# Optimization experiments

Hardware: AMD Instinct MI355X
Metric: run time of the kernel (lower is better)

## Reference

```python
import jax, jax.numpy as jnp
import numpy as np

N, E = 50000, 400000
IN_CH, HID, HEADS, EDGE_DIM = 128, 64, 4, 3
NEG_SLOPE = 0.2


def gatv2_conv(x, src, dst, edge_attr, Wl, Wr, We, att, bias):
    # x: [N, F_in]; Wl/Wr: [H*C, F_in]; We: [H*C, edge_dim]; att: [H, C]; bias: [C]
    H, C = att.shape
    n = x.shape[0]
    xl = (x @ Wl.T).reshape(n, H, C)   # source-side transform (lin_l)
    xr = (x @ Wr.T).reshape(n, H, C)   # target-side transform (lin_r)
    e = (edge_attr @ We.T).reshape(-1, H, C)
    z = jax.nn.leaky_relu(xl[src] + xr[dst] + e, NEG_SLOPE)  # [E,H,C]
    alpha = jnp.einsum('ehc,hc->eh', z, att)                 # [E,H]
    # segment softmax over incoming edges per destination node
    amax = jax.ops.segment_max(alpha, dst, num_segments=n)
    alpha = jnp.exp(alpha - amax[dst])
    denom = jax.ops.segment_sum(alpha, dst, num_segments=n)
    alpha = alpha / (denom[dst] + 1e-16)
    msg = xl[src] * alpha[:, :, None]                        # [E,H,C]
    out = jax.ops.segment_sum(msg, dst, num_segments=n)      # [N,H,C]
    return out.mean(axis=1) + bias                           # concat=False -> head mean


def setup_inputs() -> dict:
    key = jax.random.key(0)
    ks = jax.random.split(key, 16)
    s = 0.1
    return {
        'x': jax.random.normal(ks[0], (N, IN_CH), jnp.float32),
        'edge_index': jax.random.randint(ks[1], (2, E), 0, N, jnp.int32),
        'edge_attr': jax.random.normal(ks[2], (E, EDGE_DIM), jnp.float32),
        'Wl1': jax.random.normal(ks[3], (HEADS * HID, IN_CH), jnp.float32) * s,
        'Wr1': jax.random.normal(ks[4], (HEADS * HID, IN_CH), jnp.float32) * s,
        'We1': jax.random.normal(ks[5], (HEADS * HID, EDGE_DIM), jnp.float32) * s,
        'att1': jax.random.normal(ks[6], (HEADS, HID), jnp.float32) * s,
        'b1': jnp.zeros((HID,), jnp.float32),
        'Wl2': jax.random.normal(ks[7], (HEADS * HID, HID), jnp.float32) * s,
        'Wr2': jax.random.normal(ks[8], (HEADS * HID, HID), jnp.float32) * s,
        'We2': jax.random.normal(ks[9], (HEADS * HID, EDGE_DIM), jnp.float32) * s,
        'att2': jax.random.normal(ks[10], (HEADS, HID), jnp.float32) * s,
        'b2': jnp.zeros((HID,), jnp.float32),
        'prelu_w': jnp.full((HID,), 0.25, jnp.float32),
    }


def reference(x, edge_index, edge_attr, Wl1, Wr1, We1, att1, b1, Wl2, Wr2, We2, att2, b2, prelu_w):
    src, dst = edge_index[0], edge_index[1]
    h = gatv2_conv(x, src, dst, edge_attr, Wl1, Wr1, We1, att1, b1)
    h = gatv2_conv(h, src, dst, edge_attr, Wl2, Wr2, We2, att2, b2)
    return jnp.where(h >= 0, h, prelu_w * h)  # PReLU, per-channel weight
```

## Files before the change

kernel.cpp:

```cpp
#include <hip/hip_runtime.h>
#include <hip/hip_bf16.h>

#define HC 256

typedef __attribute__((ext_vector_type(8))) short bf16x8;
typedef __attribute__((ext_vector_type(4))) float f32x4;
typedef __attribute__((ext_vector_type(2))) float f32x2;

__device__ __forceinline__ void gl_lds16(const void* g, void* l) {
  __builtin_amdgcn_global_load_lds(
      (const __attribute__((address_space(1))) unsigned int*)g,
      (__attribute__((address_space(3))) unsigned int*)l, 16, 0, 0);
}

__device__ __forceinline__ void cast_w_one(const float* Wl, const float* Wr,
                                           ushort* WT, int F, int idx) {
  int col = idx / F, f = idx - col * F;
  float v = (col < 256) ? Wl[col * F + f] : Wr[(col - 256) * F + f];
  __hip_bfloat16 h = __float2bfloat16(v);
  WT[(size_t)col * F + f] = *(ushort*)&h;
}

__global__ void k_weights_hist(const float* __restrict__ Wl1, const float* __restrict__ Wr1,
                               ushort* __restrict__ WT1, const float* __restrict__ Wl2,
                               const float* __restrict__ Wr2, ushort* __restrict__ WT2,
                               const int* __restrict__ ei, int* __restrict__ deg, int E_) {
  int idx = blockIdx.x * blockDim.x + threadIdx.x;
  const int t1 = 512 * 128, t2 = 512 * 64;
  if (idx < t1) {
    cast_w_one(Wl1, Wr1, WT1, 128, idx);
  } else if (idx < t1 + t2) {
    cast_w_one(Wl2, Wr2, WT2, 64, idx - t1);
  } else {
    int e = idx - t1 - t2;
    if (e < E_) atomicAdd(&deg[ei[E_ + e]], 1);
  }
}

template <int F>
__global__ __launch_bounds__(256) void gemm_mfma(const ushort* __restrict__ A,
                                                 const ushort* __restrict__ WT,
                                                 ushort* __restrict__ xlb,
                                                 ushort* __restrict__ xrb, int n_nodes) {
  constexpr int NSTEP = F / 64;
  constexpr int SM = (2 * NSTEP * 8192 > 17408) ? 2 * NSTEP * 8192 : 17408;
  __shared__ __align__(16) ushort smem[SM];
  const int tid = threadIdx.x;
  const int wv = tid >> 6, lane = tid & 63;
  const int m16 = lane & 15, quad = lane >> 4;
  const int col0 = blockIdx.x * 128;
  const int row0 = blockIdx.y * 128;
  const int wm = (wv >> 1) * 64, wn = (wv & 1) * 64;

  f32x4 acc[4][4];
#pragma unroll
  for (int i = 0; i < 4; ++i)
#pragma unroll
    for (int j = 0; j < 4; ++j) acc[i][j] = (f32x4){0.f, 0.f, 0.f, 0.f};

  auto load_step = [&](int s) {
    ushort* As = smem + s * 16384;
    ushort* Bs = As + 8192;
    const int khat = s * 64;
#pragma unroll
    for (int t = 0; t < 4; ++t) {
      const int sl16 = tid + 256 * t;
      const int row = sl16 >> 3, sl = sl16 & 7;
      const int gch = sl ^ (row & 7);
      const int grow = row0 + row;
      if (grow < n_nodes)
        gl_lds16(A + (size_t)grow * F + khat + gch * 8, As + sl16 * 8);
      gl_lds16(WT + (size_t)(col0 + row) * F + khat + gch * 8, Bs + sl16 * 8);
    }
  };

  auto mfma_step = [&](int s) {
    ushort* As = smem + s * 16384;
    ushort* Bs = As + 8192;
#pragma unroll
    for (int kh = 0; kh < 2; ++kh) {
      bf16x8 af[4], bf[4];
#pragma unroll
      for (int i = 0; i < 4; ++i) {
        const int row = wm + i * 16 + m16;
        const int slot = (kh * 4 + quad) ^ (row & 7);
        af[i] = *(bf16x8*)&As[row * 64 + slot * 8];
      }
#pragma unroll
      for (int j = 0; j < 4; ++j) {
        const int col = wn + j * 16 + m16;
        const int slot = (kh * 4 + quad) ^ (col & 7);
        bf[j] = *(bf16x8*)&Bs[col * 64 + slot * 8];
      }
#pragma unroll
      for (int i = 0; i < 4; ++i)
#pragma unroll
        for (int j = 0; j < 4; ++j)
          acc[i][j] =
              __builtin_amdgcn_mfma_f32_16x16x32_bf16(af[i], bf[j], acc[i][j], 0, 0, 0);
    }
  };

  load_step(0);
  __syncthreads();
  if (NSTEP > 1) load_step(1);
  mfma_step(0);
  if (NSTEP > 1) {
    __syncthreads();
    mfma_step(1);
  }

  __syncthreads();
  ushort* Ct = smem;
#pragma unroll
  for (int i = 0; i < 4; ++i) {
#pragma unroll
    for (int r = 0; r < 4; ++r) {
      const int row = wm + i * 16 + quad * 4 + r;
#pragma unroll
      for (int j = 0; j < 4; ++j) {
        __hip_bfloat16 h = __float2bfloat16(acc[i][j][r]);
        Ct[row * 136 + wn + j * 16 + m16] = *(ushort*)&h;
      }
    }
  }
  __syncthreads();
  const bool is_xl = (col0 < 256);
  ushort* dst = is_xl ? xlb : xrb;
  const int cb = is_xl ? col0 : (col0 - 256);
  const int chunk = tid & 15;
#pragma unroll
  for (int it = 0; it < 8; ++it) {
    const int row = (tid >> 4) + 16 * it;
    const int grow = row0 + row;
    int4 v = *(int4*)&Ct[row * 136 + chunk * 8];
    if (grow < n_nodes)
      *(int4*)(dst + (size_t)grow * 256 + cb + chunk * 8) = v;
  }
}

__global__ void k_scan_local(const int* __restrict__ deg, int* __restrict__ rowstart,
                             int* __restrict__ partial, int n) {
  __shared__ int a[256], b[256];
  const int t = threadIdx.x;
  const int i = blockIdx.x * 256 + t;
  const int v = (i < n) ? deg[i] : 0;
  a[t] = v;
  __syncthreads();
  int* cur = a;
  int* nxt = b;
  for (int off = 1; off < 256; off <<= 1) {
    int x = cur[t];
    if (t >= off) x += cur[t - off];
    nxt[t] = x;
    __syncthreads();
    int* tmp = cur; cur = nxt; nxt = tmp;
  }
  const int incl = cur[t];
  if (i < n) rowstart[i] = incl - v;
  if (t == 255) partial[blockIdx.x] = incl;
}

__global__ void k_scan_partial(int* __restrict__ partial, int nblk,
                               float4* __restrict__ sea, int E_) {
  __shared__ int a[256], b[256];
  const int t = threadIdx.x;
  if (t < 8) sea[E_ + t] = make_float4(0.f, 0.f, 0.f, 0.f);
  const int v = (t < nblk) ? partial[t] : 0;
  a[t] = v;
  __syncthreads();
  int* cur = a;
  int* nxt = b;
  for (int off = 1; off < 256; off <<= 1) {
    int x = cur[t];
    if (t >= off) x += cur[t - off];
    nxt[t] = x;
    __syncthreads();
    int* tmp = cur; cur = nxt; nxt = tmp;
  }
  if (t < nblk) partial[t] = cur[t] - v;
}

__global__ void k_add_off(int* __restrict__ rowstart, int* __restrict__ cursor,
                          const int* __restrict__ partial, int n, int E_) {
  int i = blockIdx.x * blockDim.x + threadIdx.x;
  if (i < n) {
    int v = rowstart[i] + partial[i >> 8];
    rowstart[i] = v;
    cursor[i] = v;
  }
  if (i == 0) rowstart[n] = E_;
}

__global__ void k_prep(const float* __restrict__ x, ushort* __restrict__ A,
                       const int* __restrict__ ei, const float* __restrict__ ea,
                       int* __restrict__ cursor, float4* __restrict__ sea,
                       int n, int E_) {
  const int nx8 = n * 16;
  int idx = blockIdx.x * blockDim.x + threadIdx.x;
  if (idx < nx8) {
    const float4* xp = (const float4*)x + (size_t)idx * 2;
    float4 v0 = xp[0], v1 = xp[1];
    float vv[8] = {v0.x, v0.y, v0.z, v0.w, v1.x, v1.y, v1.z, v1.w};
    __align__(16) ushort hb[8];
#pragma unroll
    for (int j = 0; j < 8; ++j) {
      __hip_bfloat16 h = __float2bfloat16(vv[j]);
      hb[j] = *(ushort*)&h;
    }
    *(int4*)(A + (size_t)idx * 8) = *(int4*)hb;
  } else {
    int e = idx - nx8;
    if (e < E_) {
      int dst = ei[E_ + e];
      int pos = atomicAdd(&cursor[dst], 1);
      sea[pos] = make_float4(ea[e * 3], ea[e * 3 + 1], ea[e * 3 + 2],
                             __int_as_float(ei[e]));
    }
  }
}

__device__ __forceinline__ f32x2 vmax2(f32x2 a, f32x2 b) {
  return (f32x2){fmaxf(a.x, b.x), fmaxf(a.y, b.y)};
}
__device__ __forceinline__ f32x2 vmin2(f32x2 a, f32x2 b) {
  return (f32x2){fminf(a.x, b.x), fminf(a.y, b.y)};
}

__device__ __forceinline__ void edge_step(
    const ushort4& lu, const float4& eav, const f32x2* we0, const f32x2* we1,
    const f32x2* we2, const f32x2* at, const f32x2* xrl, f32x2& num01,
    f32x2& num23, float& den) {
  f32x2 lav0, lav1;
  lav0.x = __uint_as_float((unsigned)lu.x << 16);
  lav0.y = __uint_as_float((unsigned)lu.y << 16);
  lav1.x = __uint_as_float((unsigned)lu.z << 16);
  lav1.y = __uint_as_float((unsigned)lu.w << 16);
  const f32x2 zero = {0.f, 0.f};
  const f32x2 slope = {0.2f, 0.2f};
  f32x2 pv = zero;
#pragma unroll
  for (int j = 0; j < 2; ++j) {
    f32x2 la = (j == 0) ? lav0 : lav1;
    f32x2 ev = we0[j] * eav.x + we1[j] * eav.y + we2[j] * eav.z;
    f32x2 s = la + xrl[j] + ev;
    f32x2 z = vmax2(s, zero) + slope * vmin2(s, zero);
    pv = pv + z * at[j];
  }
  float p = pv.x + pv.y;
  p += __shfl_xor(p, 1);
  p += __shfl_xor(p, 2);
  p += __shfl_xor(p, 4);
  p += __shfl_xor(p, 8);
  const float w = __expf(p);
  den += w;
  num01 = num01 + (f32x2){w, w} * lav0;
  num23 = num23 + (f32x2){w, w} * lav1;
}

template <int MODE>
__global__ __launch_bounds__(64) void fused_attn(
    const ushort* __restrict__ xlb, const ushort* __restrict__ xrb,
    const int* __restrict__ rowstart, const float4* __restrict__ sea,
    const float* __restrict__ We, const float* __restrict__ att,
    const float* __restrict__ bias, const float* __restrict__ pw,
    float* __restrict__ out, ushort* __restrict__ outs, int n, int chunk) {
  const int lane = threadIdx.x;
  const int d0 = blockIdx.x * chunk;
  if (d0 >= n) return;
  const int d1 = min(d0 + chunk, n);

  f32x2 we0[2], we1[2], we2[2], at[2];
#pragma unroll
  for (int j = 0; j < 4; ++j) {
    int r = 4 * lane + j;
    ((float*)we0)[j] = We[r * 3 + 0];
    ((float*)we1)[j] = We[r * 3 + 1];
    ((float*)we2)[j] = We[r * 3 + 2];
    ((float*)at)[j] = att[r];
  }
  const float4 bias4 = ((const float4*)bias)[lane & 15];
  float4 pw4 = {0.f, 0.f, 0.f, 0.f};
  if (MODE == 1) pw4 = ((const float4*)pw)[lane & 15];
  const ushort4* xlb4 = (const ushort4*)xlb;

  for (int d = d0; d < d1; ++d) {
    const ushort4 xu = ((const ushort4*)xrb)[(unsigned)(d * 64) + lane];
    f32x2 xrl[2];
    xrl[0].x = __uint_as_float((unsigned)xu.x << 16);
    xrl[0].y = __uint_as_float((unsigned)xu.y << 16);
    xrl[1].x = __uint_as_float((unsigned)xu.z << 16);
    xrl[1].y = __uint_as_float((unsigned)xu.w << 16);

    int pos = rowstart[d];
    const int end = rowstart[d + 1];
    f32x2 num01 = {0.f, 0.f}, num23 = {0.f, 0.f};
    float den = 0.f;

    if (pos < end) {
      float4 e0 = sea[pos], e1 = sea[pos + 1], e2 = sea[pos + 2], e3 = sea[pos + 3];
      ushort4 g0 = xlb4[(unsigned)(__float_as_int(e0.w) * 64) + lane];
      ushort4 g1 = xlb4[(unsigned)(__float_as_int(e1.w) * 64) + lane];
      ushort4 g2 = xlb4[(unsigned)(__float_as_int(e2.w) * 64) + lane];
      ushort4 g3 = xlb4[(unsigned)(__float_as_int(e3.w) * 64) + lane];

      while (pos + 4 <= end) {
        ushort4 h0 = g0, h1 = g1, h2 = g2, h3 = g3;
        float4 f0 = e0, f1 = e1, f2 = e2, f3 = e3;
        if (pos + 4 < end) {
          f0 = sea[pos + 4];
          f1 = sea[pos + 5];
          f2 = sea[pos + 6];
          f3 = sea[pos + 7];
          h0 = xlb4[(unsigned)(__float_as_int(f0.w) * 64) + lane];
          h1 = xlb4[(unsigned)(__float_as_int(f1.w) * 64) + lane];
          h2 = xlb4[(unsigned)(__float_as_int(f2.w) * 64) + lane];
          h3 = xlb4[(unsigned)(__float_as_int(f3.w) * 64) + lane];
        }
        edge_step(g0, e0, we0, we1, we2, at, xrl, num01, num23, den);
        edge_step(g1, e1, we0, we1, we2, at, xrl, num01, num23, den);
        edge_step(g2, e2, we0, we1, we2, at, xrl, num01, num23, den);
        edge_step(g3, e3, we0, we1, we2, at, xrl, num01, num23, den);
        g0 = h0; g1 = h1; g2 = h2; g3 = h3;
        e0 = f0; e1 = f1; e2 = f2; e3 = f3;
        pos += 4;
      }
      const int rem = end - pos;
      if (rem > 0) edge_step(g0, e0, we0, we1, we2, at, xrl, num01, num23, den);
      if (rem > 1) edge_step(g1, e1, we0, we1, we2, at, xrl, num01, num23, den);
      if (rem > 2) edge_step(g2, e2, we0, we1, we2, at, xrl, num01, num23, den);
    }

    const float inv = 1.f / (den + 1e-16f);
    float4 r;
    r.x = num01.x * inv;
    r.y = num01.y * inv;
    r.z = num23.x * inv;
    r.w = num23.y * inv;
    r.x += __shfl_xor(r.x, 16);
    r.y += __shfl_xor(r.y, 16);
    r.z += __shfl_xor(r.z, 16);
    r.w += __shfl_xor(r.w, 16);
    r.x += __shfl_xor(r.x, 32);
    r.y += __shfl_xor(r.y, 32);
    r.z += __shfl_xor(r.z, 32);
    r.w += __shfl_xor(r.w, 32);
    if (lane < 16) {
      float o[4];
      o[0] = 0.25f * r.x + bias4.x;
      o[1] = 0.25f * r.y + bias4.y;
      o[2] = 0.25f * r.z + bias4.z;
      o[3] = 0.25f * r.w + bias4.w;
      if (MODE == 1) {
        const float pwv[4] = {pw4.x, pw4.y, pw4.z, pw4.w};
#pragma unroll
        for (int j = 0; j < 4; ++j) o[j] = (o[j] >= 0.f) ? o[j] : pwv[j] * o[j];
        ((float4*)out)[(size_t)d * 16 + lane] = make_float4(o[0], o[1], o[2], o[3]);
      } else {
        ushort hb[4];
#pragma unroll
        for (int j = 0; j < 4; ++j) {
          __hip_bfloat16 h = __float2bfloat16(o[j]);
          hb[j] = *(ushort*)&h;
        }
        *(ushort4*)(outs + (size_t)d * 64 + 4 * lane) =
            make_ushort4(hb[0], hb[1], hb[2], hb[3]);
      }
    }
  }
}

extern "C" void kernel_launch(void* const* d_in, const int* in_sizes, int n_in,
                              void* d_out, int out_size, void* d_ws, size_t ws_size,
                              hipStream_t stream) {
  const float* x    = (const float*)d_in[0];
  const int*   ei   = (const int*)d_in[1];
  const float* ea   = (const float*)d_in[2];
  const float* Wl1  = (const float*)d_in[3];
  const float* Wr1  = (const float*)d_in[4];
  const float* We1  = (const float*)d_in[5];
  const float* att1 = (const float*)d_in[6];
  const float* b1   = (const float*)d_in[7];
  const float* Wl2  = (const float*)d_in[8];
  const float* Wr2  = (const float*)d_in[9];
  const float* We2  = (const float*)d_in[10];
  const float* att2 = (const float*)d_in[11];
  const float* b2   = (const float*)d_in[12];
  const float* pw   = (const float*)d_in[13];
  const int N_ = in_sizes[0] / 128;
  const int E_ = in_sizes[1] / 2;
  float* out = (float*)d_out;

  char* w = (char*)d_ws;
  auto alloc = [&](size_t bytes) {
    char* p = w;
    w += (bytes + 255) & ~size_t(255);
    return p;
  };
  ushort* xlb      = (ushort*)alloc((size_t)N_ * 256 * 2);
  ushort* xrb      = (ushort*)alloc((size_t)N_ * 256 * 2);
  ushort* Ax       = (ushort*)alloc((size_t)N_ * 128 * 2);
  ushort* h2       = (ushort*)alloc((size_t)N_ * 64 * 2);
  float4* sea      = (float4*)alloc((size_t)(E_ + 8) * 16);
  int*    deg      = (int*)alloc((size_t)N_ * 4);
  int*    rowstart = (int*)alloc((size_t)(N_ + 1) * 4);
  int*    cursor   = (int*)alloc((size_t)N_ * 4);
  int*    partial  = (int*)alloc(256 * 4);
  ushort* WT1      = (ushort*)alloc((size_t)512 * 128 * 2);
  ushort* WT2      = (ushort*)alloc((size_t)512 * 64 * 2);

  hipMemsetAsync(deg, 0, (size_t)N_ * 4, stream);
  const int wtot = 512 * 128 + 512 * 64 + E_;
  k_weights_hist<<<(wtot + 255) / 256, 256, 0, stream>>>(Wl1, Wr1, WT1, Wl2, Wr2, WT2,
                                                         ei, deg, E_);

  const int nblk = (N_ + 255) / 256;
  k_scan_local<<<nblk, 256, 0, stream>>>(deg, rowstart, partial, N_);
  k_scan_partial<<<1, 256, 0, stream>>>(partial, nblk, sea, E_);
  k_add_off<<<nblk, 256, 0, stream>>>(rowstart, cursor, partial, N_, E_);
  const int ptot = N_ * 16 + E_;
  k_prep<<<(ptot + 255) / 256, 256, 0, stream>>>(x, Ax, ei, ea, cursor, sea, N_, E_);

  const dim3 GG(4, (N_ + 127) / 128);
  const int chunk = 2;
  const int FB = (N_ + chunk - 1) / chunk;

  gemm_mfma<128><<<GG, 256, 0, stream>>>(Ax, WT1, xlb, xrb, N_);
  fused_attn<0><<<FB, 64, 0, stream>>>(xlb, xrb, rowstart, sea, We1, att1,
                                       b1, pw, nullptr, h2, N_, chunk);
  gemm_mfma<64><<<GG, 256, 0, stream>>>(h2, WT2, xlb, xrb, N_);
  fused_attn<1><<<FB, 64, 0, stream>>>(xlb, xrb, rowstart, sea, We2, att2,
                                       b2, pw, out, nullptr, N_, chunk);
}
```

Before: 270.3 us.

## Stream edges across destination boundaries in fused attention with continuous prefetch

Reworks the fused attention kernel so a block walks one continuous stream of edges covering all its destinations. Each destination is finalized inline when the edge position reaches its row end, instead of draining and restarting the 4-deep gather pipeline per destination. Row starts are loaded once per block and broadcast with shuffles, and the next destination's xr row is prefetched. The per-block destination chunk is raised from 2 to 4, which gives fewer blocks with longer serial work and more divergent control flow around finalization.

```diff
diff --git a/kernel.cpp b/kernel.cpp
--- a/kernel.cpp
+++ b/kernel.cpp
@@ -227,6 +227,13 @@
   return (f32x2){fminf(a.x, b.x), fminf(a.y, b.y)};
 }
 
+__device__ __forceinline__ void expand_xr(const ushort4& xu, f32x2* xrl) {
+  xrl[0].x = __uint_as_float((unsigned)xu.x << 16);
+  xrl[0].y = __uint_as_float((unsigned)xu.y << 16);
+  xrl[1].x = __uint_as_float((unsigned)xu.z << 16);
+  xrl[1].y = __uint_as_float((unsigned)xu.w << 16);
+}
+
 __device__ __forceinline__ void edge_step(
     const ushort4& lu, const float4& eav, const f32x2* we0, const f32x2* we1,
     const f32x2* we2, const f32x2* at, const f32x2* xrl, f32x2& num01,
@@ -269,6 +276,7 @@
   const int d0 = blockIdx.x * chunk;
   if (d0 >= n) return;
   const int d1 = min(d0 + chunk, n);
+  const int nd = d1 - d0;
 
   f32x2 we0[2], we1[2], we2[2], at[2];
 #pragma unroll
@@ -283,91 +291,97 @@
   float4 pw4 = {0.f, 0.f, 0.f, 0.f};
   if (MODE == 1) pw4 = ((const float4*)pw)[lane & 15];
   const ushort4* xlb4 = (const ushort4*)xlb;
-
-  for (int d = d0; d < d1; ++d) {
-    const ushort4 xu = ((const ushort4*)xrb)[(unsigned)(d * 64) + lane];
-    f32x2 xrl[2];
-    xrl[0].x = __uint_as_float((unsigned)xu.x << 16);
-    xrl[0].y = __uint_as_float((unsigned)xu.y << 16);
-    xrl[1].x = __uint_as_float((unsigned)xu.z << 16);
-    xrl[1].y = __uint_as_float((unsigned)xu.w << 16);
-
-    int pos = rowstart[d];
-    const int end = rowstart[d + 1];
-    f32x2 num01 = {0.f, 0.f}, num23 = {0.f, 0.f};
-    float den = 0.f;
-
-    if (pos < end) {
-      float4 e0 = sea[pos], e1 = sea[pos + 1], e2 = sea[pos + 2], e3 = sea[pos + 3];
-      ushort4 g0 = xlb4[(unsigned)(__float_as_int(e0.w) * 64) + lane];
-      ushort4 g1 = xlb4[(unsigned)(__float_as_int(e1.w) * 64) + lane];
-      ushort4 g2 = xlb4[(unsigned)(__float_as_int(e2.w) * 64) + lane];
-      ushort4 g3 = xlb4[(unsigned)(__float_as_int(e3.w) * 64) + lane];
-
-      while (pos + 4 <= end) {
-        ushort4 h0 = g0, h1 = g1, h2 = g2, h3 = g3;
-        float4 f0 = e0, f1 = e1, f2 = e2, f3 = e3;
-        if (pos + 4 < end) {
-          f0 = sea[pos + 4];
-          f1 = sea[pos + 5];
-          f2 = sea[pos + 6];
-          f3 = sea[pos + 7];
-          h0 = xlb4[(unsigned)(__float_as_int(f0.w) * 64) + lane];
-          h1 = xlb4[(unsigned)(__float_as_int(f1.w) * 64) + lane];
-          h2 = xlb4[(unsigned)(__float_as_int(f2.w) * 64) + lane];
-          h3 = xlb4[(unsigned)(__float_as_int(f3.w) * 64) + lane];
+  const ushort4* xrb4 = (const ushort4*)xrb;
+
+  int rsv = 0;
+  if (lane <= nd) rsv = rowstart[d0 + lane];
+  int d = d0;
+  int pos = __shfl(rsv, 0);
+  const int fin = __shfl(rsv, nd);
+  int end_cur = __shfl(rsv, 1);
+
+  f32x2 xrl[2];
+  {
+    ushort4 xu0 = xrb4[(unsigned)(d0 * 64) + lane];
+    expand_xr(xu0, xrl);
+  }
+  ushort4 xu_nxt = xrb4[(unsigned)(min(d0 + 1, n - 1) * 64) + lane];
+  int d_pref = d0 + 2;
+
+  f32x2 num01 = {0.f, 0.f}, num23 = {0.f, 0.f};
+  float den = 0.f;
+
+#define FINALIZE_DST()                                                        \
+  do {                                                                        \
+    const float inv = 1.f / (den + 1e-16f);                                   \
+    float4 r;                                                                 \
+    r.x = num01.x * inv; r.y = num01.y * inv;                                 \
+    r.z = num23.x * inv; r.w = num23.y * inv;                                 \
+    r.x += __shfl_xor(r.x, 16); r.y += __shfl_xor(r.y, 16);                   \
+    r.z += __shfl_xor(r.z, 16); r.w += __shfl_xor(r.w, 16);                   \
+    r.x += __shfl_xor(r.x, 32); r.y += __shfl_xor(r.y, 32);                   \
+    r.z += __shfl_xor(r.z, 32); r.w += __shfl_xor(r.w, 32);                   \
+    if (lane < 16) {                                                          \
+      float o[4];                                                             \
+      o[0] = 0.25f * r.x + bias4.x; o[1] = 0.25f * r.y + bias4.y;             \
+      o[2] = 0.25f * r.z + bias4.z; o[3] = 0.25f * r.w + bias4.w;             \
+      if (MODE == 1) {                                                        \
+        const float pwv[4] = {pw4.x, pw4.y, pw4.z, pw4.w};                    \
+        _Pragma("unroll")                                                     \
+        for (int j = 0; j < 4; ++j) o[j] = (o[j] >= 0.f) ? o[j] : pwv[j] * o[j]; \
+        ((float4*)out)[(size_t)d * 16 + lane] = make_float4(o[0], o[1], o[2], o[3]); \
+      } else {                                                                \
+        ushort hb[4];                                                         \
+        _Pragma("unroll")                                                     \
+        for (int j = 0; j < 4; ++j) {                                         \
+          __hip_bfloat16 hh = __float2bfloat16(o[j]);                         \
+          hb[j] = *(ushort*)&hh;                                              \
+        }                                                                     \
+        *(ushort4*)(outs + (size_t)d * 64 + 4 * lane) =                       \
+            make_ushort4(hb[0], hb[1], hb[2], hb[3]);                         \
+      }                                                                       \
+    }                                                                         \
+    num01 = (f32x2){0.f, 0.f}; num23 = (f32x2){0.f, 0.f}; den = 0.f;          \
+    ++d;                                                                      \
+    end_cur = __shfl(rsv, d - d0 + 1);                                        \
+    expand_xr(xu_nxt, xrl);                                                   \
+    xu_nxt = xrb4[(unsigned)(min(d_pref, n - 1) * 64) + lane];                \
+    ++d_pref;                                                                 \
+  } while (0)
+
+  if (pos < fin) {
+    float4 e[4];
+    ushort4 g[4];
+#pragma unroll
+    for (int k = 0; k < 4; ++k) e[k] = sea[pos + k];
+#pragma unroll
+    for (int k = 0; k < 4; ++k)
+      g[k] = xlb4[(unsigned)(__float_as_int(e[k].w) * 64) + lane];
+
+    while (pos < fin) {
+      float4 f_[4];
+      ushort4 h_[4];
+#pragma unroll
+      for (int k = 0; k < 4; ++k) f_[k] = sea[pos + 4 + k];
+#pragma unroll
+      for (int k = 0; k < 4; ++k)
+        h_[k] = xlb4[(unsigned)(__float_as_int(f_[k].w) * 64) + lane];
+
+#pragma unroll
+      for (int k = 0; k < 4; ++k) {
+        const int p = pos + k;
+        if (p < fin) {
+          while (p == end_cur) FINALIZE_DST();
+          edge_step(g[k], e[k], we0, we1, we2, at, xrl, num01, num23, den);
         }
-        edge_step(g0, e0, we0, we1, we2, at, xrl, num01, num23, den);
-        edge_step(g1, e1, we0, we1, we2, at, xrl, num01, num23, den);
-        edge_step(g2, e2, we0, we1, we2, at, xrl, num01, num23, den);
-        edge_step(g3, e3, we0, we1, we2, at, xrl, num01, num23, den);
-        g0 = h0; g1 = h1; g2 = h2; g3 = h3;
-        e0 = f0; e1 = f1; e2 = f2; e3 = f3;
-        pos += 4;
       }
-      const int rem = end - pos;
-      if (rem > 0) edge_step(g0, e0, we0, we1, we2, at, xrl, num01, num23, den);
-      if (rem > 1) edge_step(g1, e1, we0, we1, we2, at, xrl, num01, num23, den);
-      if (rem > 2) edge_step(g2, e2, we0, we1, we2, at, xrl, num01, num23, den);
-    }
-
-    const float inv = 1.f / (den + 1e-16f);
-    float4 r;
-    r.x = num01.x * inv;
-    r.y = num01.y * inv;
-    r.z = num23.x * inv;
-    r.w = num23.y * inv;
-    r.x += __shfl_xor(r.x, 16);
-    r.y += __shfl_xor(r.y, 16);
-    r.z += __shfl_xor(r.z, 16);
-    r.w += __shfl_xor(r.w, 16);
-    r.x += __shfl_xor(r.x, 32);
-    r.y += __shfl_xor(r.y, 32);
-    r.z += __shfl_xor(r.z, 32);
-    r.w += __shfl_xor(r.w, 32);
-    if (lane < 16) {
-      float o[4];
-      o[0] = 0.25f * r.x + bias4.x;
-      o[1] = 0.25f * r.y + bias4.y;
-      o[2] = 0.25f * r.z + bias4.z;
-      o[3] = 0.25f * r.w + bias4.w;
-      if (MODE == 1) {
-        const float pwv[4] = {pw4.x, pw4.y, pw4.z, pw4.w};
-#pragma unroll
-        for (int j = 0; j < 4; ++j) o[j] = (o[j] >= 0.f) ? o[j] : pwv[j] * o[j];
-        ((float4*)out)[(size_t)d * 16 + lane] = make_float4(o[0], o[1], o[2], o[3]);
-      } else {
-        ushort hb[4];
-#pragma unroll
-        for (int j = 0; j < 4; ++j) {
-          __hip_bfloat16 h = __float2bfloat16(o[j]);
-          hb[j] = *(ushort*)&h;
-        }
-        *(ushort4*)(outs + (size_t)d * 64 + 4 * lane) =
-            make_ushort4(hb[0], hb[1], hb[2], hb[3]);
-      }
-    }
-  }
+#pragma unroll
+      for (int k = 0; k < 4; ++k) { g[k] = h_[k]; e[k] = f_[k]; }
+      pos += 4;
+    }
+  }
+  while (d < d1) FINALIZE_DST();
+#undef FINALIZE_DST
 }
 
 extern "C" void kernel_launch(void* const* d_in, const int* in_sizes, int n_in,
@@ -422,7 +436,7 @@
   k_prep<<<(ptot + 255) / 256, 256, 0, stream>>>(x, Ax, ei, ea, cursor, sea, N_, E_);
 
   const dim3 GG(4, (N_ + 127) / 128);
-  const int chunk = 2;
+  const int chunk = 4;
   const int FB = (N_ + chunk - 1) / chunk;
 
   gemm_mfma<128><<<GG, 256, 0, stream>>>(Ax, WT1, xlb, xrb, N_);
```

Result: slower. 304.3 us (+12.6%).

## Rewrite leaky-ReLU attention algebraically, use DPP reductions, merge scan kernels

Applied to the files above, without the earlier changes.

Leaky ReLU times att is rewritten as 0.6*s + 0.4*|s| with log2(e) folded into the att weights, so the softmax weight comes from exp2f instead of __expf. The 16-lane butterfly reduction moves from shfl_xor to DPP row_ror adds, which avoids LDS-backed shuffles. The single-block partial scan and the add-offset kernel are merged into one kernel in which every block redoes the small partial scan, removing one launch. The edge inner loop gets fewer ops, at the cost of slightly different float rounding.

```diff
diff --git a/kernel.cpp b/kernel.cpp
--- a/kernel.cpp
+++ b/kernel.cpp
@@ -161,11 +161,11 @@
   if (t == 255) partial[blockIdx.x] = incl;
 }
 
-__global__ void k_scan_partial(int* __restrict__ partial, int nblk,
-                               float4* __restrict__ sea, int E_) {
+__global__ void k_scan_final(const int* __restrict__ partial, int nblk,
+                             int* __restrict__ rowstart, int* __restrict__ cursor,
+                             float4* __restrict__ sea, int n, int E_) {
   __shared__ int a[256], b[256];
   const int t = threadIdx.x;
-  if (t < 8) sea[E_ + t] = make_float4(0.f, 0.f, 0.f, 0.f);
   const int v = (t < nblk) ? partial[t] : 0;
   a[t] = v;
   __syncthreads();
@@ -178,18 +178,15 @@
     __syncthreads();
     int* tmp = cur; cur = nxt; nxt = tmp;
   }
-  if (t < nblk) partial[t] = cur[t] - v;
-}
-
-__global__ void k_add_off(int* __restrict__ rowstart, int* __restrict__ cursor,
-                          const int* __restrict__ partial, int n, int E_) {
-  int i = blockIdx.x * blockDim.x + threadIdx.x;
+  const int boff = (blockIdx.x > 0) ? cur[blockIdx.x - 1] : 0;
+  const int i = blockIdx.x * 256 + t;
   if (i < n) {
-    int v = rowstart[i] + partial[i >> 8];
-    rowstart[i] = v;
-    cursor[i] = v;
+    int vv = rowstart[i] + boff;
+    rowstart[i] = vv;
+    cursor[i] = vv;
   }
   if (i == 0) rowstart[n] = E_;
+  if (blockIdx.x == 0 && t < 8) sea[E_ + t] = make_float4(0.f, 0.f, 0.f, 0.f);
 }
 
 __global__ void k_prep(const float* __restrict__ x, ushort* __restrict__ A,
@@ -220,39 +217,42 @@
   }
 }
 
-__device__ __forceinline__ f32x2 vmax2(f32x2 a, f32x2 b) {
-  return (f32x2){fmaxf(a.x, b.x), fmaxf(a.y, b.y)};
-}
-__device__ __forceinline__ f32x2 vmin2(f32x2 a, f32x2 b) {
-  return (f32x2){fminf(a.x, b.x), fminf(a.y, b.y)};
+__device__ __forceinline__ float dpp_ror_add(float p) {
+  p += __int_as_float(__builtin_amdgcn_update_dpp(
+      0, __float_as_int(p), 0x128, 0xF, 0xF, true));
+  p += __int_as_float(__builtin_amdgcn_update_dpp(
+      0, __float_as_int(p), 0x124, 0xF, 0xF, true));
+  p += __int_as_float(__builtin_amdgcn_update_dpp(
+      0, __float_as_int(p), 0x122, 0xF, 0xF, true));
+  p += __int_as_float(__builtin_amdgcn_update_dpp(
+      0, __float_as_int(p), 0x121, 0xF, 0xF, true));
+  return p;
 }
 
 __device__ __forceinline__ void edge_step(
     const ushort4& lu, const float4& eav, const f32x2* we0, const f32x2* we1,
-    const f32x2* we2, const f32x2* at, const f32x2* xrl, f32x2& num01,
-    f32x2& num23, float& den) {
+    const f32x2* we2, const f32x2* at6, const f32x2* at4, const f32x2* xrl,
+    f32x2& num01, f32x2& num23, float& den) {
   f32x2 lav0, lav1;
   lav0.x = __uint_as_float((unsigned)lu.x << 16);
   lav0.y = __uint_as_float((unsigned)lu.y << 16);
   lav1.x = __uint_as_float((unsigned)lu.z << 16);
   lav1.y = __uint_as_float((unsigned)lu.w << 16);
-  const f32x2 zero = {0.f, 0.f};
-  const f32x2 slope = {0.2f, 0.2f};
-  f32x2 pv = zero;
+  f32x2 pv = {0.f, 0.f};
 #pragma unroll
   for (int j = 0; j < 2; ++j) {
     f32x2 la = (j == 0) ? lav0 : lav1;
-    f32x2 ev = we0[j] * eav.x + we1[j] * eav.y + we2[j] * eav.z;
-    f32x2 s = la + xrl[j] + ev;
-    f32x2 z = vmax2(s, zero) + slope * vmin2(s, zero);
-    pv = pv + z * at[j];
+    f32x2 t = xrl[j] + we0[j] * eav.x;
+    t = t + we1[j] * eav.y;
+    t = t + we2[j] * eav.z;
+    f32x2 s = t + la;
+    f32x2 sa = {fabsf(s.x), fabsf(s.y)};
+    pv = pv + at6[j] * s;
+    pv = pv + at4[j] * sa;
   }
   float p = pv.x + pv.y;
-  p += __shfl_xor(p, 1);
-  p += __shfl_xor(p, 2);
-  p += __shfl_xor(p, 4);
-  p += __shfl_xor(p, 8);
-  const float w = __expf(p);
+  p = dpp_ror_add(p);
+  const float w = exp2f(p);
   den += w;
   num01 = num01 + (f32x2){w, w} * lav0;
   num23 = num23 + (f32x2){w, w} * lav1;
@@ -270,14 +270,17 @@
   if (d0 >= n) return;
   const int d1 = min(d0 + chunk, n);
 
-  f32x2 we0[2], we1[2], we2[2], at[2];
+  f32x2 we0[2], we1[2], we2[2], at6[2], at4[2];
+  const float L2E = 1.4426950408889634f;
 #pragma unroll
   for (int j = 0; j < 4; ++j) {
     int r = 4 * lane + j;
     ((float*)we0)[j] = We[r * 3 + 0];
     ((float*)we1)[j] = We[r * 3 + 1];
     ((float*)we2)[j] = We[r * 3 + 2];
-    ((float*)at)[j] = att[r];
+    float a = att[r];
+    ((float*)at6)[j] = a * (0.6f * L2E);
+    ((float*)at4)[j] = a * (0.4f * L2E);
   }
   const float4 bias4 = ((const float4*)bias)[lane & 15];
   float4 pw4 = {0.f, 0.f, 0.f, 0.f};
@@ -317,18 +320,18 @@
           h2 = xlb4[(unsigned)(__float_as_int(f2.w) * 64) + lane];
           h3 = xlb4[(unsigned)(__float_as_int(f3.w) * 64) + lane];
         }
-        edge_step(g0, e0, we0, we1, we2, at, xrl, num01, num23, den);
-        edge_step(g1, e1, we0, we1, we2, at, xrl, num01, num23, den);
-        edge_step(g2, e2, we0, we1, we2, at, xrl, num01, num23, den);
-        edge_step(g3, e3, we0, we1, we2, at, xrl, num01, num23, den);
+        edge_step(g0, e0, we0, we1, we2, at6, at4, xrl, num01, num23, den);
+        edge_step(g1, e1, we0, we1, we2, at6, at4, xrl, num01, num23, den);
+        edge_step(g2, e2, we0, we1, we2, at6, at4, xrl, num01, num23, den);
+        edge_step(g3, e3, we0, we1, we2, at6, at4, xrl, num01, num23, den);
         g0 = h0; g1 = h1; g2 = h2; g3 = h3;
         e0 = f0; e1 = f1; e2 = f2; e3 = f3;
         pos += 4;
       }
       const int rem = end - pos;
-      if (rem > 0) edge_step(g0, e0, we0, we1, we2, at, xrl, num01, num23, den);
-      if (rem > 1) edge_step(g1, e1, we0, we1, we2, at, xrl, num01, num23, den);
-      if (rem > 2) edge_step(g2, e2, we0, we1, we2, at, xrl, num01, num23, den);
+      if (rem > 0) edge_step(g0, e0, we0, we1, we2, at6, at4, xrl, num01, num23, den);
+      if (rem > 1) edge_step(g1, e1, we0, we1, we2, at6, at4, xrl, num01, num23, den);
+      if (rem > 2) edge_step(g2, e2, we0, we1, we2, at6, at4, xrl, num01, num23, den);
     }
 
     const float inv = 1.f / (den + 1e-16f);
@@ -416,8 +419,7 @@
 
   const int nblk = (N_ + 255) / 256;
   k_scan_local<<<nblk, 256, 0, stream>>>(deg, rowstart, partial, N_);
-  k_scan_partial<<<1, 256, 0, stream>>>(partial, nblk, sea, E_);
-  k_add_off<<<nblk, 256, 0, stream>>>(rowstart, cursor, partial, N_, E_);
+  k_scan_final<<<nblk, 256, 0, stream>>>(partial, nblk, rowstart, cursor, sea, N_, E_);
   const int ptot = N_ * 16 + E_;
   k_prep<<<(ptot + 255) / 256, 256, 0, stream>>>(x, Ax, ei, ea, cursor, sea, N_, E_);
 
```

Result: faster. 261.3 us (-3.3%).
